# Kernel optimization log

Hardware: AMD Instinct MI355X
Metric: run time of the kernel (lower is better)

Reference implementation:

```python
import jax, jax.numpy as jnp
import numpy as np

H = 16          # hidden_size
L = 24          # num_layers
LEN_TRAIN = 96
LEN_PRED = 48
B = 256         # leading dim of input (acts as TIME axis for the LSTMs, see notes)


def setup_inputs() -> dict:
    key = jax.random.key(0)
    ks = jax.random.split(key, 16)
    s = 1.0 / np.sqrt(H)  # PyTorch LSTM/Linear init scale
    u = lambda k, shp: jax.random.uniform(k, shp, jnp.float32, -s, s)
    return {
        "x": jax.random.normal(ks[0], (B, 1, LEN_TRAIN), jnp.float32),
        # lstm1: layer0 input_size=1, layers 1..23 input_size=2H
        "W_ih0_1": u(ks[1], (2, 4 * H, 1)),
        "W_ih_1": u(ks[2], (L - 1, 2, 4 * H, 2 * H)),
        "W_hh_1": u(ks[3], (L, 2, 4 * H, H)),
        "b_ih_1": u(ks[4], (L, 2, 4 * H)),
        "b_hh_1": u(ks[5], (L, 2, 4 * H)),
        # lstm2: all layers input_size=2H
        "W_ih_2": u(ks[6], (L, 2, 4 * H, 2 * H)),
        "W_hh_2": u(ks[7], (L, 2, 4 * H, H)),
        "b_ih_2": u(ks[8], (L, 2, 4 * H)),
        "b_hh_2": u(ks[9], (L, 2, 4 * H)),
        "fc1_w": u(ks[10], (1000, 2 * LEN_PRED * H)),
        "fc1_b": u(ks[11], (1000,)),
        "fc2_w": u(ks[12], (LEN_PRED, 1000)),
        "fc2_b": u(ks[13], (LEN_PRED,)),
    }


def _lstm_dir(x, Wih, Whh, bih, bhh, reverse):
    # x: (T, N, in). Precompute input-gate GEMM over whole sequence.
    xg = jnp.einsum("tni,gi->tng", x, Wih) + bih + bhh  # (T, N, 4H)

    def step(carry, g_in):
        h, c = carry
        g = g_in + h @ Whh.T
        i, f, gg, o = jnp.split(g, 4, axis=-1)  # PyTorch gate order i,f,g,o
        c = jax.nn.sigmoid(f) * c + jax.nn.sigmoid(i) * jnp.tanh(gg)
        h = jax.nn.sigmoid(o) * jnp.tanh(c)
        return (h, c), h

    N = x.shape[1]
    init = (jnp.zeros((N, H), x.dtype), jnp.zeros((N, H), x.dtype))
    _, hs = jax.lax.scan(step, init, xg, reverse=reverse)
    return hs  # (T, N, H), in original time order


def _bilstm_stack(x, Wih_per_layer, Whh, bih, bhh):
    for l in range(Whh.shape[0]):
        Wih = Wih_per_layer[l]
        fwd = _lstm_dir(x, Wih[0], Whh[l, 0], bih[l, 0], bhh[l, 0], False)
        bwd = _lstm_dir(x, Wih[1], Whh[l, 1], bih[l, 1], bhh[l, 1], True)
        x = jnp.concatenate([fwd, bwd], axis=-1)  # (T, N, 2H)
    return x


def reference(x, W_ih0_1, W_ih_1, W_hh_1, b_ih_1, b_hh_1,
              W_ih_2, W_hh_2, b_ih_2, b_hh_2,
              fc1_w, fc1_b, fc2_w, fc2_b):
    xp = jnp.transpose(x, (0, 2, 1))  # (B, 96, 1); dim0 is the LSTM time axis (batch_first=False quirk)
    wih1 = [W_ih0_1] + [W_ih_1[i] for i in range(L - 1)]
    h = _bilstm_stack(xp, wih1, W_hh_1, b_ih_1, b_hh_1)      # (B, 96, 2H)
    x1 = h[:, -LEN_PRED:, :]                                  # (B, 48, 2H)
    wih2 = [W_ih_2[i] for i in range(L)]
    h2 = _bilstm_stack(x1, wih2, W_hh_2, b_ih_2, b_hh_2)      # (B, 48, 2H)
    z = h2 + x1
    flat = z.reshape(z.shape[0], -1)                          # (B, 1536)
    y = jax.nn.relu(flat @ fc1_w.T + fc1_b) @ fc2_w.T + fc2_b # (B, 48)
    return jnp.transpose(y.reshape(y.shape[0], LEN_PRED, 1), (0, 2, 1))  # (B, 1, 48)
```

## Files before the change

### kernel.cpp

```cpp
#include <hip/hip_runtime.h>


template <int SEL>
__device__ __forceinline__ float quad_bcast(float v) {
  return __int_as_float(__builtin_amdgcn_update_dpp(
      0, __float_as_int(v), SEL * 0x55, 0xF, 0xF, true));
}

__global__ __launch_bounds__(256) void lstm_chain(
    const float* __restrict__ x, const float* __restrict__ W_ih0_1,
    const float* __restrict__ W_ih_1, const float* __restrict__ W_hh_1,
    const float* __restrict__ b_ih_1, const float* __restrict__ b_hh_1,
    const float* __restrict__ W_ih_2, const float* __restrict__ W_hh_2,
    const float* __restrict__ b_ih_2, const float* __restrict__ b_hh_2,
    float* __restrict__ x1g, float* __restrict__ h2g) {
  __shared__ float xgF[256 * 64];
  __shared__ float xgB[256 * 64];

  const int tid = threadIdx.x;
  const int lane = tid & 63;
  const int w = tid >> 6;
  const int n = blockIdx.x;
  const int nlay = (n < 48) ? 24 : 48;

  for (int L = 0; L < nlay; ++L) {
    const bool s2 = (L >= 24);
    const int l = s2 ? (L - 24) : L;
    const float* bih = s2 ? b_ih_2 : b_ih_1;
    const float* bhh = s2 ? b_hh_2 : b_hh_1;
    const float biasF = bih[l * 128 + lane] + bhh[l * 128 + lane];
    const float biasB = bih[l * 128 + 64 + lane] + bhh[l * 128 + 64 + lane];

    const int jj = lane >> 2, g = lane & 3;
    const int r = g * 16 + jj;
    float whh[16];
    if (w < 2) {
      const float* Whh =
          s2 ? (W_hh_2 + (size_t)l * 2048) : (W_hh_1 + (size_t)l * 2048);
      const float* wp = Whh + ((size_t)w * 64 + r) * 16;
#pragma unroll
      for (int k = 0; k < 16; ++k) whh[k] = wp[k];
    }

    if (L == 0) {
      xgF[tid * 64 + 32] = x[(size_t)tid * 96 + n];
      const float w0F = W_ih0_1[lane];
      const float w0B = W_ih0_1[64 + lane];
      __syncthreads();
      for (int ti = 0; ti < 64; ++ti) {
        const int t = w * 64 + ti;
        const float xs = xgF[t * 64 + 32];
        xgF[t * 64 + lane] = fmaf(w0F, xs, biasF);
        xgB[t * 64 + lane] = fmaf(w0B, xs, biasB);
      }
    } else {
      const float* Wih = s2 ? (W_ih_2 + (size_t)l * 4096)
                            : (W_ih_1 + (size_t)(l - 1) * 4096);
      float wf[32], wb[32];
      {
        const float4* wpF =
            reinterpret_cast<const float4*>(Wih + (size_t)lane * 32);
        const float4* wpB =
            reinterpret_cast<const float4*>(Wih + (size_t)(64 + lane) * 32);
#pragma unroll
        for (int q = 0; q < 8; ++q) {
          const float4 a = wpF[q];
          wf[4 * q + 0] = a.x; wf[4 * q + 1] = a.y;
          wf[4 * q + 2] = a.z; wf[4 * q + 3] = a.w;
          const float4 b = wpB[q];
          wb[4 * q + 0] = b.x; wb[4 * q + 1] = b.y;
          wb[4 * q + 2] = b.z; wb[4 * q + 3] = b.w;
        }
      }
      for (int ti = 0; ti < 64; ++ti) {
        const int t = w * 64 + ti;
        const float4* hf4 = reinterpret_cast<const float4*>(&xgF[t * 64 + 32]);
        const float4* hb4 = reinterpret_cast<const float4*>(&xgB[t * 64 + 48]);
        float4 in[8];
#pragma unroll
        for (int q = 0; q < 4; ++q) in[q] = hf4[q];
#pragma unroll
        for (int q = 0; q < 4; ++q) in[4 + q] = hb4[q];
        float a0 = biasF, a1 = 0.f, a2 = 0.f, a3 = 0.f;
        float c0 = biasB, c1 = 0.f, c2 = 0.f, c3 = 0.f;
#pragma unroll
        for (int q = 0; q < 8; ++q) {
          const float4 v = in[q];
          a0 = fmaf(wf[4 * q + 0], v.x, a0);
          a1 = fmaf(wf[4 * q + 1], v.y, a1);
          a2 = fmaf(wf[4 * q + 2], v.z, a2);
          a3 = fmaf(wf[4 * q + 3], v.w, a3);
          c0 = fmaf(wb[4 * q + 0], v.x, c0);
          c1 = fmaf(wb[4 * q + 1], v.y, c1);
          c2 = fmaf(wb[4 * q + 2], v.z, c2);
          c3 = fmaf(wb[4 * q + 3], v.w, c3);
        }
        xgF[t * 64 + lane] = (a0 + a1) + (a2 + a3);
        xgB[t * 64 + lane] = (c0 + c1) + (c2 + c3);
      }
    }
    __syncthreads();

    if (w < 2) {
      const float s_ = (g == 2) ? 2.885390082f : -1.442695041f;
      const float m_ = (g == 2) ? -2.0f : 1.0f;
      const float b_ = (g == 2) ? 1.0f : 0.0f;
      float hs[16];
#pragma unroll
      for (int k = 0; k < 16; ++k) hs[k] = 0.f;
      float c = 0.f;

#define LSTM_STEP(XG, CUR, TT, HCOL)                                      \
  {                                                                       \
    float a0 = (CUR), a1 = 0.f, a2 = 0.f, a3 = 0.f;                       \
    _Pragma("unroll") for (int k = 0; k < 16; k += 4) {                   \
      a0 = fmaf(whh[k + 0], hs[k + 0], a0);                               \
      a1 = fmaf(whh[k + 1], hs[k + 1], a1);                               \
      a2 = fmaf(whh[k + 2], hs[k + 2], a2);                               \
      a3 = fmaf(whh[k + 3], hs[k + 3], a3);                               \
    }                                                                     \
    const float gv = (a0 + a1) + (a2 + a3);                               \
    const float e = __builtin_amdgcn_exp2f(s_ * gv);                      \
    const float v = fmaf(m_, __builtin_amdgcn_rcpf(1.0f + e), b_);        \
    const float si = quad_bcast<0>(v);                                    \
    const float sf = quad_bcast<1>(v);                                    \
    const float tg = quad_bcast<2>(v);                                    \
    const float so = quad_bcast<3>(v);                                    \
    c = fmaf(sf, c, si * tg);                                             \
    const float e2 = __builtin_amdgcn_exp2f(2.885390082f * c);            \
    const float th = fmaf(-2.0f, __builtin_amdgcn_rcpf(1.0f + e2), 1.0f); \
    const float h = so * th;                                              \
    if (g == 0) XG[(TT)*64 + (HCOL)] = h;                                 \
    const int hbb = __float_as_int(h);                                    \
    _Pragma("unroll") for (int k = 0; k < 16; ++k) hs[k] =                \
        __int_as_float(__builtin_amdgcn_readlane(hbb, 4 * k));            \
  }

#define SCAN_LOOP(XG, DT, T0, HCOL)                                       \
  {                                                                       \
    int t = (T0);                                                         \
    float cur0 = XG[t * 64 + r];                                          \
    float cur1 = XG[(t + (DT)) * 64 + r];                                 \
    for (int tt = 0; tt < 256; tt += 2) {                                 \
      const float nx0 = XG[((t + 2 * (DT)) & 255) * 64 + r];              \
      LSTM_STEP(XG, cur0, t, HCOL)                                        \
      const float nx1 = XG[((t + 3 * (DT)) & 255) * 64 + r];              \
      LSTM_STEP(XG, cur1, t + (DT), HCOL)                                 \
      cur0 = nx0;                                                         \
      cur1 = nx1;                                                         \
      t += 2 * (DT);                                                      \
    }                                                                     \
  }

      if (w == 0) {
        SCAN_LOOP(xgF, 1, 0, 32 + jj)
      } else {
        SCAN_LOOP(xgB, -1, 255, 48 + jj)
      }
#undef SCAN_LOOP
#undef LSTM_STEP
    }
    __syncthreads();

    if ((L == 23 && n >= 48) || L == 47) {
      float* dst = (L == 23) ? x1g : h2g;
#pragma unroll
      for (int p = 0; p < 8; ++p) {
        const int idx = p * 256 + tid;
        const int t = idx >> 3, q = idx & 7;
        const float4 v =
            (q < 4) ? *reinterpret_cast<const float4*>(&xgF[t * 64 + 32 + q * 4])
                    : *reinterpret_cast<const float4*>(
                          &xgB[t * 64 + 48 + (q - 4) * 4]);
        *reinterpret_cast<float4*>(dst + (size_t)t * 1536 + (n - 48) * 32 +
                                   q * 4) = v;
      }
      __syncthreads();
    }
  }
}

__global__ __launch_bounds__(256) void fc1_kernel(
    const float* __restrict__ h2,
    const float* __restrict__ x1,
    const float* __restrict__ w1, const float* __restrict__ b1,
    float* __restrict__ y1) {
  __shared__ float Zs[16][68];
  __shared__ float Ws[16][68];
  const int tid = threadIdx.x;
  const int m0 = blockIdx.x * 64;
  const int b0 = blockIdx.y * 64;
  const int rr = tid >> 2;
  const int c4 = (tid & 3) * 4;
  const int tx = tid & 15, ty = tid >> 4;

  float acc[4][4];
#pragma unroll
  for (int i = 0; i < 4; ++i)
#pragma unroll
    for (int jj = 0; jj < 4; ++jj) acc[i][jj] = 0.f;

  const bool wvalid = (m0 + rr) < 1000;
  const float* zr = h2 + (size_t)(b0 + rr) * 1536 + c4;
  const float* zr2 = x1 + (size_t)(b0 + rr) * 1536 + c4;
  const float* wr = w1 + (size_t)(m0 + rr) * 1536 + c4;

  float4 za = *reinterpret_cast<const float4*>(zr);
  float4 zb = *reinterpret_cast<const float4*>(zr2);
  float4 wv = wvalid ? *reinterpret_cast<const float4*>(wr)
                     : make_float4(0.f, 0.f, 0.f, 0.f);

  for (int k0 = 0; k0 < 1536; k0 += 16) {
    Zs[c4 + 0][rr] = za.x + zb.x;
    Zs[c4 + 1][rr] = za.y + zb.y;
    Zs[c4 + 2][rr] = za.z + zb.z;
    Zs[c4 + 3][rr] = za.w + zb.w;
    Ws[c4 + 0][rr] = wv.x;
    Ws[c4 + 1][rr] = wv.y;
    Ws[c4 + 2][rr] = wv.z;
    Ws[c4 + 3][rr] = wv.w;
    if (k0 + 16 < 1536) {
      za = *reinterpret_cast<const float4*>(zr + k0 + 16);
      zb = *reinterpret_cast<const float4*>(zr2 + k0 + 16);
      if (wvalid) wv = *reinterpret_cast<const float4*>(wr + k0 + 16);
    }
    __syncthreads();
#pragma unroll
    for (int kk = 0; kk < 16; ++kk) {
      const float4 av = *reinterpret_cast<const float4*>(&Zs[kk][ty * 4]);
      const float4 bv = *reinterpret_cast<const float4*>(&Ws[kk][tx * 4]);
      const float a_[4] = {av.x, av.y, av.z, av.w};
      const float b_[4] = {bv.x, bv.y, bv.z, bv.w};
#pragma unroll
      for (int i = 0; i < 4; ++i)
#pragma unroll
        for (int jj = 0; jj < 4; ++jj)
          acc[i][jj] = fmaf(a_[i], b_[jj], acc[i][jj]);
    }
    __syncthreads();
  }
#pragma unroll
  for (int i = 0; i < 4; ++i) {
    const int b = b0 + ty * 4 + i;
#pragma unroll
    for (int jj = 0; jj < 4; ++jj) {
      const int m = m0 + tx * 4 + jj;
      if (m < 1000) {
        const float vo = acc[i][jj] + b1[m];
        y1[(size_t)b * 1000 + m] = vo > 0.f ? vo : 0.f;
      }
    }
  }
}

__global__ __launch_bounds__(64) void fc2_kernel(
    const float* __restrict__ y1, const float* __restrict__ w2,
    const float* __restrict__ b2, float* __restrict__ out) {
  __shared__ float ys[1000];
  const int b = blockIdx.x;
  for (int k = threadIdx.x; k < 1000; k += 64) ys[k] = y1[(size_t)b * 1000 + k];
  __syncthreads();
  const int p = threadIdx.x;
  if (p < 48) {
    float a0 = b2[p], a1 = 0.f, a2 = 0.f, a3 = 0.f;
    const float* wr = w2 + (size_t)p * 1000;
    for (int k = 0; k < 1000; k += 4) {
      const float4 wv = *reinterpret_cast<const float4*>(wr + k);
      a0 = fmaf(ys[k + 0], wv.x, a0);
      a1 = fmaf(ys[k + 1], wv.y, a1);
      a2 = fmaf(ys[k + 2], wv.z, a2);
      a3 = fmaf(ys[k + 3], wv.w, a3);
    }
    out[(size_t)b * 48 + p] = (a0 + a1) + (a2 + a3);
  }
}

extern "C" void kernel_launch(void* const* d_in, const int* in_sizes, int n_in,
                              void* d_out, int out_size, void* d_ws,
                              size_t ws_size, hipStream_t stream) {
  const float* x = (const float*)d_in[0];
  const float* W_ih0_1 = (const float*)d_in[1];
  const float* W_ih_1 = (const float*)d_in[2];
  const float* W_hh_1 = (const float*)d_in[3];
  const float* b_ih_1 = (const float*)d_in[4];
  const float* b_hh_1 = (const float*)d_in[5];
  const float* W_ih_2 = (const float*)d_in[6];
  const float* W_hh_2 = (const float*)d_in[7];
  const float* b_ih_2 = (const float*)d_in[8];
  const float* b_hh_2 = (const float*)d_in[9];
  const float* fc1_w = (const float*)d_in[10];
  const float* fc1_b = (const float*)d_in[11];
  const float* fc2_w = (const float*)d_in[12];
  const float* fc2_b = (const float*)d_in[13];

  float* ws = (float*)d_ws;
  float* x1g = ws;
  float* h2g = ws + 393216;
  float* y1 = ws + 786432;

  lstm_chain<<<96, 256, 0, stream>>>(x, W_ih0_1, W_ih_1, W_hh_1, b_ih_1,
                                     b_hh_1, W_ih_2, W_hh_2, b_ih_2, b_hh_2,
                                     x1g, h2g);
  fc1_kernel<<<dim3(16, 4), 256, 0, stream>>>(h2g, x1g, fc1_w, fc1_b, y1);
  fc2_kernel<<<256, 64, 0, stream>>>(y1, fc2_w, fc2_b, (float*)d_out);
}
```

Baseline: 2.632 ms.

## Remap LSTM recurrence lanes to row-rotate DPP matvec with swizzled gate exchange

Reorganizes the recurrent step so each lane computes two gate rows, using DPP row-rotate to share h within 16-lane rows instead of 16 readlane broadcasts. Gate pre-activations are stored in an interleaved column layout so each lane loads a float2. Gate combination uses a ds_swizzle across half-wavefronts. The aim is a shorter serial dependency chain per timestep, at the cost of an extra LDS swizzle and a more intricate lane mapping.

```diff
diff --git a/kernel.cpp b/kernel.cpp
--- a/kernel.cpp
+++ b/kernel.cpp
@@ -1,10 +1,15 @@
 #include <hip/hip_runtime.h>
 
 
-template <int SEL>
-__device__ __forceinline__ float quad_bcast(float v) {
+template <int K>
+__device__ __forceinline__ float row_ror(float v) {
   return __int_as_float(__builtin_amdgcn_update_dpp(
-      0, __float_as_int(v), SEL * 0x55, 0xF, 0xF, true));
+      0, __float_as_int(v), 0x120 | K, 0xF, 0xF, true));
+}
+
+__device__ __forceinline__ float swz16(float v) {
+  return __int_as_float(
+      __builtin_amdgcn_ds_swizzle(__float_as_int(v), 0x401F));
 }
 
 __global__ __launch_bounds__(256) void lstm_chain(
@@ -23,6 +28,14 @@
   const int n = blockIdx.x;
   const int nlay = (n < 48) ? 24 : 48;
 
+  const int lh = lane & 31;
+  const int j16 = lane & 15;
+  const bool low = (lane & 16) == 0;
+  const float s2_ = low ? 2.885390082f : -1.442695041f;
+  const float m2_ = low ? -2.0f : 1.0f;
+  const float c2_ = low ? 1.0f : 0.0f;
+  const int pcol = 2 * lh + (lane >> 5);
+
   for (int L = 0; L < nlay; ++L) {
     const bool s2 = (L >= 24);
     const int l = s2 ? (L - 24) : L;
@@ -31,15 +44,16 @@
     const float biasF = bih[l * 128 + lane] + bhh[l * 128 + lane];
     const float biasB = bih[l * 128 + 64 + lane] + bhh[l * 128 + 64 + lane];
 
-    const int jj = lane >> 2, g = lane & 3;
-    const int r = g * 16 + jj;
-    float whh[16];
+    float w1[16], w2[16];
     if (w < 2) {
       const float* Whh =
           s2 ? (W_hh_2 + (size_t)l * 2048) : (W_hh_1 + (size_t)l * 2048);
-      const float* wp = Whh + ((size_t)w * 64 + r) * 16;
-#pragma unroll
-      for (int k = 0; k < 16; ++k) whh[k] = wp[k];
+#pragma unroll
+      for (int k = 0; k < 16; ++k) {
+        const int ks = (j16 - k) & 15;
+        w1[k] = Whh[((size_t)w * 64 + lh) * 16 + ks];
+        w2[k] = Whh[((size_t)w * 64 + lh + 32) * 16 + ks];
+      }
     }
 
     if (L == 0) {
@@ -50,8 +64,8 @@
       for (int ti = 0; ti < 64; ++ti) {
         const int t = w * 64 + ti;
         const float xs = xgF[t * 64 + 32];
-        xgF[t * 64 + lane] = fmaf(w0F, xs, biasF);
-        xgB[t * 64 + lane] = fmaf(w0B, xs, biasB);
+        xgF[t * 64 + pcol] = fmaf(w0F, xs, biasF);
+        xgB[t * 64 + pcol] = fmaf(w0B, xs, biasB);
       }
     } else {
       const float* Wih = s2 ? (W_ih_2 + (size_t)l * 4096)
@@ -95,57 +109,64 @@
           c2 = fmaf(wb[4 * q + 2], v.z, c2);
           c3 = fmaf(wb[4 * q + 3], v.w, c3);
         }
-        xgF[t * 64 + lane] = (a0 + a1) + (a2 + a3);
-        xgB[t * 64 + lane] = (c0 + c1) + (c2 + c3);
+        xgF[t * 64 + pcol] = (a0 + a1) + (a2 + a3);
+        xgB[t * 64 + pcol] = (c0 + c1) + (c2 + c3);
       }
     }
     __syncthreads();
 
     if (w < 2) {
-      const float s_ = (g == 2) ? 2.885390082f : -1.442695041f;
-      const float m_ = (g == 2) ? -2.0f : 1.0f;
-      const float b_ = (g == 2) ? 1.0f : 0.0f;
-      float hs[16];
-#pragma unroll
-      for (int k = 0; k < 16; ++k) hs[k] = 0.f;
-      float c = 0.f;
-
-#define LSTM_STEP(XG, CUR, TT, HCOL)                                      \
+      float hreg = 0.f, creg = 0.f;
+
+#define MVK(K, AA, BB)                          \
+  {                                             \
+    const float rk_ = row_ror<K>(hreg);         \
+    AA = fmaf(w1[K], rk_, AA);                  \
+    BB = fmaf(w2[K], rk_, BB);                  \
+  }
+
+#define LSTM_STEP(XG, CUR, TT, TCOL)                                      \
   {                                                                       \
-    float a0 = (CUR), a1 = 0.f, a2 = 0.f, a3 = 0.f;                       \
-    _Pragma("unroll") for (int k = 0; k < 16; k += 4) {                   \
-      a0 = fmaf(whh[k + 0], hs[k + 0], a0);                               \
-      a1 = fmaf(whh[k + 1], hs[k + 1], a1);                               \
-      a2 = fmaf(whh[k + 2], hs[k + 2], a2);                               \
-      a3 = fmaf(whh[k + 3], hs[k + 3], a3);                               \
-    }                                                                     \
-    const float gv = (a0 + a1) + (a2 + a3);                               \
-    const float e = __builtin_amdgcn_exp2f(s_ * gv);                      \
-    const float v = fmaf(m_, __builtin_amdgcn_rcpf(1.0f + e), b_);        \
-    const float si = quad_bcast<0>(v);                                    \
-    const float sf = quad_bcast<1>(v);                                    \
-    const float tg = quad_bcast<2>(v);                                    \
-    const float so = quad_bcast<3>(v);                                    \
-    c = fmaf(sf, c, si * tg);                                             \
-    const float e2 = __builtin_amdgcn_exp2f(2.885390082f * c);            \
-    const float th = fmaf(-2.0f, __builtin_amdgcn_rcpf(1.0f + e2), 1.0f); \
-    const float h = so * th;                                              \
-    if (g == 0) XG[(TT)*64 + (HCOL)] = h;                                 \
-    const int hbb = __float_as_int(h);                                    \
-    _Pragma("unroll") for (int k = 0; k < 16; ++k) hs[k] =                \
-        __int_as_float(__builtin_amdgcn_readlane(hbb, 4 * k));            \
-  }
-
-#define SCAN_LOOP(XG, DT, T0, HCOL)                                       \
+    float a0 = (CUR).x, a1 = 0.f, a2 = 0.f, a3 = 0.f;                     \
+    float b0 = (CUR).y, b1 = 0.f, b2 = 0.f, b3 = 0.f;                     \
+    a0 = fmaf(w1[0], hreg, a0);                                           \
+    b0 = fmaf(w2[0], hreg, b0);                                           \
+    MVK(1, a1, b1) MVK(2, a2, b2) MVK(3, a3, b3)                          \
+    MVK(4, a0, b0) MVK(5, a1, b1) MVK(6, a2, b2) MVK(7, a3, b3)           \
+    MVK(8, a0, b0) MVK(9, a1, b1) MVK(10, a2, b2) MVK(11, a3, b3)         \
+    MVK(12, a0, b0) MVK(13, a1, b1) MVK(14, a2, b2) MVK(15, a3, b3)       \
+    const float gv1 = (a0 + a1) + (a2 + a3);                              \
+    const float gv2 = (b0 + b1) + (b2 + b3);                              \
+    const float e1 = __builtin_amdgcn_exp2f(-1.442695041f * gv1);         \
+    const float A1 = __builtin_amdgcn_rcpf(1.0f + e1);                    \
+    const float e2 = __builtin_amdgcn_exp2f(s2_ * gv2);                   \
+    const float A2 = fmaf(m2_, __builtin_amdgcn_rcpf(1.0f + e2), c2_);    \
+    const float S1 = swz16(A1);                                           \
+    const float S2 = swz16(A2);                                           \
+    const float ig = low ? A1 * A2 : S1 * S2;                             \
+    const float ff = low ? S1 : A1;                                       \
+    const float oo = low ? S2 : A2;                                       \
+    creg = fmaf(ff, creg, ig);                                            \
+    const float et = __builtin_amdgcn_exp2f(2.885390082f * creg);         \
+    const float th = fmaf(-2.0f, __builtin_amdgcn_rcpf(1.0f + et), 1.0f); \
+    hreg = oo * th;                                                       \
+    if (lane < 16) XG[(TT)*64 + (TCOL) + lane] = hreg;                    \
+  }
+
+#define SCAN_LOOP(XG, DT, T0, TCOL)                                       \
   {                                                                       \
     int t = (T0);                                                         \
-    float cur0 = XG[t * 64 + r];                                          \
-    float cur1 = XG[(t + (DT)) * 64 + r];                                 \
+    float2 cur0 =                                                         \
+        *reinterpret_cast<const float2*>(&XG[t * 64 + 2 * lh]);           \
+    float2 cur1 =                                                         \
+        *reinterpret_cast<const float2*>(&XG[(t + (DT)) * 64 + 2 * lh]);  \
     for (int tt = 0; tt < 256; tt += 2) {                                 \
-      const float nx0 = XG[((t + 2 * (DT)) & 255) * 64 + r];              \
-      LSTM_STEP(XG, cur0, t, HCOL)                                        \
-      const float nx1 = XG[((t + 3 * (DT)) & 255) * 64 + r];              \
-      LSTM_STEP(XG, cur1, t + (DT), HCOL)                                 \
+      const float2 nx0 = *reinterpret_cast<const float2*>(                \
+          &XG[((t + 2 * (DT)) & 255) * 64 + 2 * lh]);                     \
+      LSTM_STEP(XG, cur0, t, TCOL)                                        \
+      const float2 nx1 = *reinterpret_cast<const float2*>(                \
+          &XG[((t + 3 * (DT)) & 255) * 64 + 2 * lh]);                     \
+      LSTM_STEP(XG, cur1, t + (DT), TCOL)                                 \
       cur0 = nx0;                                                         \
       cur1 = nx1;                                                         \
       t += 2 * (DT);                                                      \
@@ -153,12 +174,13 @@
   }
 
       if (w == 0) {
-        SCAN_LOOP(xgF, 1, 0, 32 + jj)
+        SCAN_LOOP(xgF, 1, 0, 32)
       } else {
-        SCAN_LOOP(xgB, -1, 255, 48 + jj)
+        SCAN_LOOP(xgB, -1, 255, 48)
       }
 #undef SCAN_LOOP
 #undef LSTM_STEP
+#undef MVK
     }
     __syncthreads();
 
```

After: 3.279 ms. 1.25x slower.
